# Kernel tuning notes

Hardware: AMD Instinct MI355X
Metric: run time of the kernel (lower is better)

Reference implementation:

```python
import jax, jax.numpy as jnp
import numpy as np

B, S = 64, 1000
ENC, DEC = 512, 512


def setup_inputs() -> dict:
    key = jax.random.key(0)
    k1, k2, k3, k4, k5 = jax.random.split(key, 5)
    hidden = jax.random.normal(k1, (B, DEC), dtype=jnp.float32)
    encoder_outputs = jax.random.normal(k2, (B, S, 2 * ENC), dtype=jnp.float32)
    # attn: Linear(enc_hidden_dim*2 + dec_hidden_dim -> dec_hidden_dim)
    fan_in = 2 * ENC + DEC
    bound = 1.0 / np.sqrt(fan_in)
    attn_w = jax.random.uniform(k3, (fan_in, DEC), minval=-bound, maxval=bound, dtype=jnp.float32)
    attn_b = jax.random.uniform(k4, (DEC,), minval=-bound, maxval=bound, dtype=jnp.float32)
    v = jax.random.uniform(k5, (DEC,), dtype=jnp.float32)  # torch.rand -> U[0,1)
    return {"hidden": hidden, "encoder_outputs": encoder_outputs,
            "attn_w": attn_w, "attn_b": attn_b, "v": v}


def reference(hidden, encoder_outputs, attn_w, attn_b, v):
    # hidden: [B, D], encoder_outputs: [B, S, 2E]
    S_len = encoder_outputs.shape[1]
    h_rep = jnp.broadcast_to(hidden[:, None, :], (hidden.shape[0], S_len, hidden.shape[1]))
    cat = jnp.concatenate([h_rep, encoder_outputs], axis=2)          # [B, S, D+2E]
    energy = jnp.tanh(cat @ attn_w + attn_b)                          # [B, S, D]
    attention = jnp.einsum('bsd,d->bs', energy, v)                    # [B, S]
    return jax.nn.softmax(attention, axis=1)
```

## Files before the change

kernel.cpp:

```cpp
#include <hip/hip_runtime.h>
#include <hip/hip_bf16.h>

typedef __attribute__((ext_vector_type(8))) short short8;
typedef __attribute__((ext_vector_type(4))) float float4v;

__device__ inline unsigned short f2bf(float f) {
    union { float f; unsigned int i; } c; c.f = f;
    unsigned int r = c.i + 0x7FFFu + ((c.i >> 16) & 1u);
    return (unsigned short)(r >> 16);
}

__global__ void k_transpose(const float* __restrict__ W,
                            unsigned short* __restrict__ Wt) {
    int idx = blockIdx.x * 256 + threadIdx.x;
    int d  = idx & 511;
    int kg = idx >> 9;
    short8 v;
#pragma unroll
    for (int j = 0; j < 8; j++)
        v[j] = (short)f2bf(W[(size_t)(512 + kg * 8 + j) * 512 + d]);
    *(short8*)(Wt + (size_t)d * 1024 + kg * 8) = v;
}

__global__ void k_hb(const float* __restrict__ hidden,
                     const float* __restrict__ W,
                     const float* __restrict__ bias,
                     float* __restrict__ hb) {
    int b = blockIdx.x, d = threadIdx.x;
    __shared__ float h[512];
    h[d] = hidden[b * 512 + d];
    __syncthreads();
    float a = 0.f;
#pragma unroll 8
    for (int k = 0; k < 512; k++)
        a += h[k] * W[(size_t)k * 512 + d];
    hb[b * 512 + d] = a + bias[d];
}

__launch_bounds__(256, 2)
__global__ void k_main(const float* __restrict__ enc,
                       const unsigned short* __restrict__ Wt,
                       const float* __restrict__ hb,
                       const float* __restrict__ vvec,
                       float* __restrict__ att) {
    const int b    = blockIdx.y;
    const int s0   = blockIdx.x * 64;
    const int tid  = threadIdx.x;
    const int wave = tid >> 6;
    const int lane = tid & 63;
    const int col  = lane & 15;
    const int quad = lane >> 4;

    __shared__ unsigned short As[2][64][72];

    const int r  = tid >> 2;
    const int cq = tid & 3;
    int s = s0 + r; if (s > 999) s = 999;
    const float* arow = enc + ((size_t)(b * 1000 + s) * 1024 + cq * 16);

    const unsigned short* bptr = Wt + (size_t)(wave * 128 + col) * 1024 + quad * 8;

    float4v acc[4][8];
#pragma unroll
    for (int mt = 0; mt < 4; mt++)
#pragma unroll
        for (int nt = 0; nt < 8; nt++)
            acc[mt][nt] = float4v{0.f, 0.f, 0.f, 0.f};

    float4v st[4];
#pragma unroll
    for (int j = 0; j < 4; j++) st[j] = *(const float4v*)(arow + j * 4);
    {
        short8 wv0, wv1;
#pragma unroll
        for (int j = 0; j < 4; j++) {
            wv0[j]     = (short)f2bf(st[0][j]);
            wv0[j + 4] = (short)f2bf(st[1][j]);
            wv1[j]     = (short)f2bf(st[2][j]);
            wv1[j + 4] = (short)f2bf(st[3][j]);
        }
        unsigned short* wp = &As[0][r][cq * 16];
        *(short8*)(wp)     = wv0;
        *(short8*)(wp + 8) = wv1;
    }
    __syncthreads();

    for (int c = 0; c < 16; c++) {
        const int buf = c & 1;

        if (c < 15) {
#pragma unroll
            for (int j = 0; j < 4; j++)
                st[j] = *(const float4v*)(arow + (c + 1) * 64 + j * 4);
        }

        short8 af[2][4];
#pragma unroll
        for (int ks = 0; ks < 2; ks++)
#pragma unroll
            for (int mt = 0; mt < 4; mt++)
                af[ks][mt] = *(const short8*)(&As[buf][mt * 16 + col][ks * 32 + quad * 8]);

#pragma unroll
        for (int ks = 0; ks < 2; ks++) {
            short8 bf[8];
#pragma unroll
            for (int nt = 0; nt < 8; nt++)
                bf[nt] = *(const short8*)(bptr + c * 64 + ks * 32 + (size_t)nt * 16 * 1024);
#pragma unroll
            for (int mt = 0; mt < 4; mt++)
#pragma unroll
                for (int nt = 0; nt < 8; nt++)
                    acc[mt][nt] = __builtin_amdgcn_mfma_f32_16x16x32_bf16(
                        af[ks][mt], bf[nt], acc[mt][nt], 0, 0, 0);
        }

        if (c < 15) {
            short8 wv0, wv1;
#pragma unroll
            for (int j = 0; j < 4; j++) {
                wv0[j]     = (short)f2bf(st[0][j]);
                wv0[j + 4] = (short)f2bf(st[1][j]);
                wv1[j]     = (short)f2bf(st[2][j]);
                wv1[j + 4] = (short)f2bf(st[3][j]);
            }
            unsigned short* wq = &As[buf ^ 1][r][cq * 16];
            *(short8*)(wq)     = wv0;
            *(short8*)(wq + 8) = wv1;
        }
        __syncthreads();
    }

    float vv[8], hbv[8];
#pragma unroll
    for (int nt = 0; nt < 8; nt++) {
        int d = wave * 128 + nt * 16 + col;
        vv[nt]  = vvec[d];
        hbv[nt] = hb[b * 512 + d];
    }
    float rs[4][4];
#pragma unroll
    for (int mt = 0; mt < 4; mt++)
#pragma unroll
        for (int rg = 0; rg < 4; rg++) rs[mt][rg] = 0.f;

#pragma unroll
    for (int mt = 0; mt < 4; mt++)
#pragma unroll
        for (int nt = 0; nt < 8; nt++)
#pragma unroll
            for (int rg = 0; rg < 4; rg++) {
                float e = acc[mt][nt][rg] + hbv[nt];
                float t = 1.f - 2.f / (__expf(2.f * e) + 1.f);
                rs[mt][rg] += t * vv[nt];
            }

#pragma unroll
    for (int mt = 0; mt < 4; mt++)
#pragma unroll
        for (int rg = 0; rg < 4; rg++) {
            float x = rs[mt][rg];
            x += __shfl_xor(x, 1);
            x += __shfl_xor(x, 2);
            x += __shfl_xor(x, 4);
            x += __shfl_xor(x, 8);
            rs[mt][rg] = x;
        }

    __shared__ float red[4][64];
    if (col == 0) {
#pragma unroll
        for (int mt = 0; mt < 4; mt++)
#pragma unroll
            for (int rg = 0; rg < 4; rg++)
                red[wave][mt * 16 + quad * 4 + rg] = rs[mt][rg];
    }
    __syncthreads();
    if (tid < 64) {
        float sum = red[0][tid] + red[1][tid] + red[2][tid] + red[3][tid];
        int ss = s0 + tid;
        if (ss < 1000) att[b * 1000 + ss] = sum;
    }
}

__global__ void k_softmax(const float* __restrict__ att,
                          float* __restrict__ out) {
    int b = blockIdx.x, tid = threadIdx.x;
    __shared__ float sm[4], ss[4];
    float x[4], mx = -1e30f;
#pragma unroll
    for (int i = 0; i < 4; i++) {
        int s = tid + 256 * i;
        x[i] = (s < 1000) ? att[b * 1000 + s] : -1e30f;
        mx = fmaxf(mx, x[i]);
    }
    for (int off = 1; off < 64; off <<= 1) mx = fmaxf(mx, __shfl_xor(mx, off));
    if ((tid & 63) == 0) sm[tid >> 6] = mx;
    __syncthreads();
    mx = fmaxf(fmaxf(sm[0], sm[1]), fmaxf(sm[2], sm[3]));

    float ex[4], se = 0.f;
#pragma unroll
    for (int i = 0; i < 4; i++) {
        ex[i] = __expf(x[i] - mx);
        if (tid + 256 * i >= 1000) ex[i] = 0.f;
        se += ex[i];
    }
    for (int off = 1; off < 64; off <<= 1) se += __shfl_xor(se, off);
    if ((tid & 63) == 0) ss[tid >> 6] = se;
    __syncthreads();
    se = ss[0] + ss[1] + ss[2] + ss[3];
    float inv = 1.f / se;
#pragma unroll
    for (int i = 0; i < 4; i++) {
        int s = tid + 256 * i;
        if (s < 1000) out[b * 1000 + s] = ex[i] * inv;
    }
}

extern "C" void kernel_launch(void* const* d_in, const int* in_sizes, int n_in,
                              void* d_out, int out_size, void* d_ws, size_t ws_size,
                              hipStream_t stream) {
    const float* hidden = (const float*)d_in[0];
    const float* enc    = (const float*)d_in[1];
    const float* attn_w = (const float*)d_in[2];
    const float* attn_b = (const float*)d_in[3];
    const float* v      = (const float*)d_in[4];
    float* out = (float*)d_out;

    char* ws = (char*)d_ws;
    unsigned short* Wt = (unsigned short*)ws;
    float* hb  = (float*)(ws + (1 << 20));
    float* att = (float*)(ws + (1 << 20) + (128 << 10));

    k_transpose<<<256, 256, 0, stream>>>(attn_w, Wt);
    k_hb<<<64, 512, 0, stream>>>(hidden, attn_w, attn_b, hb);
    k_main<<<dim3(16, 64), 256, 0, stream>>>(enc, Wt, hb, v, att);
    k_softmax<<<64, 256, 0, stream>>>(att, out);
}
```

Before: 480.5 us.

## Split output dimension across two blocks and pre-swizzle weights into MFMA fragment order

The main GEMM kernel now splits the 512-wide decoder dimension into two halves handled by separate blocks, which doubles the grid and halves each block's accumulator count so occupancy can rise from 2 to 3 blocks per CU. The transpose kernel stores weights in the exact per-lane fragment order, so each B-fragment load becomes a contiguous coalesced read. Partial attention scores from the two halves are written separately and summed in the softmax kernel. The cost is that every block now reads and converts the encoder tile, so the fp32 encoder traffic and conversion work are doubled.

```diff
diff --git a/kernel.cpp b/kernel.cpp
--- a/kernel.cpp
+++ b/kernel.cpp
@@ -12,14 +12,20 @@
 
 __global__ void k_transpose(const float* __restrict__ W,
                             unsigned short* __restrict__ Wt) {
-    int idx = blockIdx.x * 256 + threadIdx.x;
-    int d  = idx & 511;
-    int kg = idx >> 9;
+    int idx  = blockIdx.x * 256 + threadIdx.x;
+    int lane = idx & 63;
+    int nt   = (idx >> 6) & 3;
+    int ks   = (idx >> 8) & 1;
+    int w    = (idx >> 9) & 3;
+    int c    = (idx >> 11) & 15;
+    int dh   = (idx >> 15) & 1;
+    int d  = dh * 256 + w * 64 + nt * 16 + (lane & 15);
+    int kb = c * 64 + ks * 32 + (lane >> 4) * 8;
     short8 v;
 #pragma unroll
     for (int j = 0; j < 8; j++)
-        v[j] = (short)f2bf(W[(size_t)(512 + kg * 8 + j) * 512 + d]);
-    *(short8*)(Wt + (size_t)d * 1024 + kg * 8) = v;
+        v[j] = (short)f2bf(W[(size_t)(512 + kb + j) * 512 + d]);
+    *(short8*)(Wt + (size_t)idx * 8) = v;
 }
 
 __global__ void k_hb(const float* __restrict__ hidden,
@@ -37,14 +43,15 @@
     hb[b * 512 + d] = a + bias[d];
 }
 
-__launch_bounds__(256, 2)
+__launch_bounds__(256, 3)
 __global__ void k_main(const float* __restrict__ enc,
                        const unsigned short* __restrict__ Wt,
                        const float* __restrict__ hb,
                        const float* __restrict__ vvec,
                        float* __restrict__ att) {
-    const int b    = blockIdx.y;
-    const int s0   = blockIdx.x * 64;
+    const int dh   = blockIdx.x;
+    const int s0   = blockIdx.y * 64;
+    const int b    = blockIdx.z;
     const int tid  = threadIdx.x;
     const int wave = tid >> 6;
     const int lane = tid & 63;
@@ -58,13 +65,13 @@
     int s = s0 + r; if (s > 999) s = 999;
     const float* arow = enc + ((size_t)(b * 1000 + s) * 1024 + cq * 16);
 
-    const unsigned short* bptr = Wt + (size_t)(wave * 128 + col) * 1024 + quad * 8;
-
-    float4v acc[4][8];
-#pragma unroll
-    for (int mt = 0; mt < 4; mt++)
-#pragma unroll
-        for (int nt = 0; nt < 8; nt++)
+    const unsigned short* bbase = Wt + (size_t)dh * 262144 + wave * 4096 + lane * 8;
+
+    float4v acc[4][4];
+#pragma unroll
+    for (int mt = 0; mt < 4; mt++)
+#pragma unroll
+        for (int nt = 0; nt < 4; nt++)
             acc[mt][nt] = float4v{0.f, 0.f, 0.f, 0.f};
 
     float4v st[4];
@@ -88,31 +95,31 @@
     for (int c = 0; c < 16; c++) {
         const int buf = c & 1;
 
+        short8 bf[2][4];
+#pragma unroll
+        for (int ks = 0; ks < 2; ks++)
+#pragma unroll
+            for (int nt = 0; nt < 4; nt++)
+                bf[ks][nt] = *(const short8*)(bbase + c * 16384 + (ks * 4 + nt) * 512);
+
         if (c < 15) {
 #pragma unroll
             for (int j = 0; j < 4; j++)
                 st[j] = *(const float4v*)(arow + (c + 1) * 64 + j * 4);
         }
 
-        short8 af[2][4];
-#pragma unroll
-        for (int ks = 0; ks < 2; ks++)
+#pragma unroll
+        for (int ks = 0; ks < 2; ks++) {
+            short8 af[4];
 #pragma unroll
             for (int mt = 0; mt < 4; mt++)
-                af[ks][mt] = *(const short8*)(&As[buf][mt * 16 + col][ks * 32 + quad * 8]);
-
-#pragma unroll
-        for (int ks = 0; ks < 2; ks++) {
-            short8 bf[8];
-#pragma unroll
-            for (int nt = 0; nt < 8; nt++)
-                bf[nt] = *(const short8*)(bptr + c * 64 + ks * 32 + (size_t)nt * 16 * 1024);
+                af[mt] = *(const short8*)(&As[buf][mt * 16 + col][ks * 32 + quad * 8]);
 #pragma unroll
             for (int mt = 0; mt < 4; mt++)
 #pragma unroll
-                for (int nt = 0; nt < 8; nt++)
+                for (int nt = 0; nt < 4; nt++)
                     acc[mt][nt] = __builtin_amdgcn_mfma_f32_16x16x32_bf16(
-                        af[ks][mt], bf[nt], acc[mt][nt], 0, 0, 0);
+                        af[mt], bf[ks][nt], acc[mt][nt], 0, 0, 0);
         }
 
         if (c < 15) {
@@ -131,10 +138,10 @@
         __syncthreads();
     }
 
-    float vv[8], hbv[8];
-#pragma unroll
-    for (int nt = 0; nt < 8; nt++) {
-        int d = wave * 128 + nt * 16 + col;
+    float vv[4], hbv[4];
+#pragma unroll
+    for (int nt = 0; nt < 4; nt++) {
+        int d = dh * 256 + wave * 64 + nt * 16 + col;
         vv[nt]  = vvec[d];
         hbv[nt] = hb[b * 512 + d];
     }
@@ -147,7 +154,7 @@
 #pragma unroll
     for (int mt = 0; mt < 4; mt++)
 #pragma unroll
-        for (int nt = 0; nt < 8; nt++)
+        for (int nt = 0; nt < 4; nt++)
 #pragma unroll
             for (int rg = 0; rg < 4; rg++) {
                 float e = acc[mt][nt][rg] + hbv[nt];
@@ -179,7 +186,7 @@
     if (tid < 64) {
         float sum = red[0][tid] + red[1][tid] + red[2][tid] + red[3][tid];
         int ss = s0 + tid;
-        if (ss < 1000) att[b * 1000 + ss] = sum;
+        if (ss < 1000) att[(size_t)dh * 64000 + b * 1000 + ss] = sum;
     }
 }
 
@@ -191,7 +198,11 @@
 #pragma unroll
     for (int i = 0; i < 4; i++) {
         int s = tid + 256 * i;
-        x[i] = (s < 1000) ? att[b * 1000 + s] : -1e30f;
+        if (s < 1000) {
+            x[i] = att[b * 1000 + s] + att[64000 + b * 1000 + s];
+        } else {
+            x[i] = -1e30f;
+        }
         mx = fmaxf(mx, x[i]);
     }
     for (int off = 1; off < 64; off <<= 1) mx = fmaxf(mx, __shfl_xor(mx, off));
@@ -235,6 +246,6 @@
 
     k_transpose<<<256, 256, 0, stream>>>(attn_w, Wt);
     k_hb<<<64, 512, 0, stream>>>(hidden, attn_w, attn_b, hb);
-    k_main<<<dim3(16, 64), 256, 0, stream>>>(enc, Wt, hb, v, att);
+    k_main<<<dim3(2, 16, 64), 256, 0, stream>>>(enc, Wt, hb, v, att);
     k_softmax<<<64, 256, 0, stream>>>(att, out);
 }
```

Result: faster. 457.2 us (-4.8%).
